# Kernel optimization log

Measured on AMD Instinct MI355X. Metric: run time of the kernel, lower is better.

## Reference

```python
import jax, jax.numpy as jnp
import numpy as np

N = 100000     # nodes
E = 1600000    # edges (avg degree 16)
CI = 3         # input features (x, z, t)
W = 128        # hidden width
CO = 1         # output features
L = 4          # processor layers


def setup_inputs() -> dict:
    key = jax.random.key(0)
    ks = jax.random.split(key, 10)
    s = 0.1
    x = jax.random.normal(ks[0], (N, CI), jnp.float32)
    # compute_mask is an external geometry-dependent, no-grad mask; emulate as 0/1 node mask
    mask = (jax.random.uniform(ks[1], (N, 1)) > 0.5).astype(jnp.float32)
    edge_index = jax.random.randint(ks[2], (2, E), 0, N, dtype=jnp.int32)
    W_enc = jax.random.normal(ks[3], (CI, W), jnp.float32) * s
    b_enc = jnp.zeros((W,), jnp.float32)
    W_p = jax.random.normal(ks[4], (L, W, W), jnp.float32) * s
    b_p = jnp.zeros((L, W), jnp.float32)
    W_dec = jax.random.normal(ks[5], (W, CO), jnp.float32) * s
    b_dec = jnp.zeros((CO,), jnp.float32)
    return {"x": x, "mask": mask, "edge_index": edge_index,
            "W_enc": W_enc, "b_enc": b_enc, "W_p": W_p, "b_p": b_p,
            "W_dec": W_dec, "b_dec": b_dec}


def reference(x, mask, edge_index, W_enc, b_enc, W_p, b_p, W_dec, b_dec):
    src, dst = edge_index[0], edge_index[1]
    n = x.shape[0]
    # GCN symmetric normalization with self-loops: deg = 1 + in-degree
    deg = 1.0 + jax.ops.segment_sum(jnp.ones((src.shape[0],), x.dtype), dst, num_segments=n)
    dis = jax.lax.rsqrt(deg)                      # deg^{-1/2}, [N]
    norm = dis[src] * dis[dst]                    # [E]

    def gcn(h, Wt, b):
        h = h @ Wt                                # [N, out]
        agg = jax.ops.segment_sum(h[src] * norm[:, None], dst, num_segments=n)
        # self-loop contribution: norm_ii = dis_i^2
        return agg + h * (dis * dis)[:, None] + b

    h = jax.nn.relu(gcn(x, W_enc, b_enc))
    for l in range(L):
        h = jax.nn.relu(gcn(h, W_p[l], b_p[l]))
    out = gcn(h, W_dec, b_dec)
    return out * mask
```

## Files before the change

kernel.cpp:

```cpp
#include <hip/hip_runtime.h>
#include <hip/hip_fp16.h>


#define HW 128
#define NBMAX 1024
#define CAP 4096
#define PBLK 256

typedef _Float16 f16x8 __attribute__((ext_vector_type(8)));
typedef float f32x4 __attribute__((ext_vector_type(4)));

__global__ void k_zero_i32(int* __restrict__ a, int n) {
    int i = blockIdx.x * 256 + threadIdx.x;
    if (i < n) a[i] = 0;
}

__global__ __launch_bounds__(256) void k_histb(const int* __restrict__ dstA,
                                               int* __restrict__ bcnt,
                                               int* __restrict__ pcnt,
                                               int nb, int e, int nblk) {
    __shared__ int lh[NBMAX];
    for (int b = threadIdx.x; b < nb; b += 256) lh[b] = 0;
    __syncthreads();
    int blk = blockIdx.x;
    int c0 = (int)(((long long)e * blk) / nblk);
    int c1 = (int)(((long long)e * (blk + 1)) / nblk);
    for (int i = c0 + threadIdx.x; i < c1; i += 256) atomicAdd(&lh[dstA[i] >> 7], 1);
    __syncthreads();
    for (int b = threadIdx.x; b < nb; b += 256) {
        int v = lh[b];
        pcnt[(size_t)blk * nb + b] = v;
        if (v) atomicAdd(&bcnt[b], v);
    }
}

__global__ void k_bscan(const int* __restrict__ bcnt, int* __restrict__ bstart,
                        int nb, int etot) {
    __shared__ int s[1024];
    int t = threadIdx.x;
    int d0 = (t < nb) ? bcnt[t] : 0;
    s[t] = d0;
    __syncthreads();
    for (int off = 1; off < 1024; off <<= 1) {
        int v = (t >= off) ? s[t - off] : 0;
        __syncthreads();
        s[t] += v;
        __syncthreads();
    }
    if (t < nb) bstart[t] = s[t] - d0;
    if (t == 0) bstart[nb] = etot;
}

__global__ __launch_bounds__(PBLK) void k_soff2(const int* __restrict__ pcnt,
                                                const int* __restrict__ bstart,
                                                int* __restrict__ soff, int nb) {
    __shared__ int s[PBLK];
    int b = blockIdx.x, t = threadIdx.x;
    int v = pcnt[(size_t)t * nb + b];
    s[t] = v;
    __syncthreads();
    for (int off = 1; off < PBLK; off <<= 1) {
        int u = (t >= off) ? s[t - off] : 0;
        __syncthreads();
        s[t] += u;
        __syncthreads();
    }
    soff[(size_t)t * nb + b] = bstart[b] + s[t] - v;
}

__global__ __launch_bounds__(256) void k_part(const int* __restrict__ srcA,
                                              const int* __restrict__ dstA,
                                              const int* __restrict__ soff,
                                              unsigned* __restrict__ stage,
                                              int nb, int e, int nblk) {
    __shared__ int loff[NBMAX];
    __shared__ int lh[NBMAX];
    int blk = blockIdx.x;
    for (int b = threadIdx.x; b < nb; b += 256) {
        loff[b] = soff[(size_t)blk * nb + b];
        lh[b] = 0;
    }
    __syncthreads();
    int c0 = (int)(((long long)e * blk) / nblk);
    int c1 = (int)(((long long)e * (blk + 1)) / nblk);
    for (int i = c0 + threadIdx.x; i < c1; i += 256) {
        int d = dstA[i];
        int bk = d >> 7;
        int p = loff[bk] + atomicAdd(&lh[bk], 1);
        stage[p] = ((unsigned)srcA[i] << 7) | (unsigned)(d & 127);
    }
}

__global__ __launch_bounds__(256) void k_build(const unsigned* __restrict__ stage,
                                               const int* __restrict__ bstart,
                                               const float* __restrict__ x,
                                               int* __restrict__ row_start,
                                               float* __restrict__ dis,
                                               float4* __restrict__ x4,
                                               int* __restrict__ csr, int n, int nb) {
    __shared__ int lcnt[128];
    __shared__ int sc[128];
    __shared__ int lcsr[CAP];
    int b = blockIdx.x, tid = threadIdx.x;
    int base = bstart[b], end = bstart[b + 1], cnt = end - base;
    int node0 = b << 7;

    if (tid < 128) lcnt[tid] = 0;
    __syncthreads();
    for (int j = tid; j < cnt; j += 256) atomicAdd(&lcnt[stage[base + j] & 127], 1);
    __syncthreads();
    if (tid < 128) sc[tid] = lcnt[tid];
    __syncthreads();
    for (int off = 1; off < 128; off <<= 1) {
        int v = (tid < 128 && tid >= off) ? sc[tid - off] : 0;
        __syncthreads();
        if (tid < 128) sc[tid] += v;
        __syncthreads();
    }
    int node = node0 + tid;
    if (tid < 128 && node < n) {
        int excl = sc[tid] - lcnt[tid];
        row_start[node] = base + excl;
        float dv = rsqrtf(1.f + (float)lcnt[tid]);
        dis[node] = dv;
        x4[node] = make_float4(x[node * 3] * dv, x[node * 3 + 1] * dv,
                               x[node * 3 + 2] * dv, 0.f);
    }
    if (tid == 0 && b == nb - 1) row_start[n] = end;
    __syncthreads();
    if (tid < 128) sc[tid] = sc[tid] - lcnt[tid];
    if (tid < 128) lcnt[tid] = 0;
    __syncthreads();
    if (cnt <= CAP) {
        for (int j = tid; j < cnt; j += 256) {
            unsigned v = stage[base + j];
            int dl = v & 127;
            int p = atomicAdd(&lcnt[dl], 1);
            lcsr[sc[dl] + p] = (int)(v >> 7);
        }
        __syncthreads();
        for (int j = tid; j < cnt; j += 256) csr[base + j] = lcsr[j];
    } else {
        for (int j = tid; j < cnt; j += 256) {
            unsigned v = stage[base + j];
            int dl = v & 127;
            int p = atomicAdd(&lcnt[dl], 1);
            csr[base + sc[dl] + p] = (int)(v >> 7);
        }
    }
}

__global__ void k_prep_wt(const float* __restrict__ Wp, __half* __restrict__ WTh,
                          __half* __restrict__ WTl, int total) {
    int t = blockIdx.x * 256 + threadIdx.x;
    if (t >= total) return;
    int l = t >> 14;
    int kc = t & 16383;
    int k = kc >> 7, c = kc & 127;
    float w = Wp[t];
    __half hi = __float2half_rn(w);
    __half lo = __float2half_rn(w - __half2float(hi));
    size_t o = ((size_t)l << 14) + (size_t)c * HW + k;
    WTh[o] = hi;
    WTl[o] = lo;
}

__global__ void k_enc_agg(const float4* __restrict__ x4, const int* __restrict__ rs,
                          const int* __restrict__ csr, const float* __restrict__ dis,
                          float4* __restrict__ zx, int n) {
    int i = blockIdx.x * 256 + threadIdx.x;
    if (i >= n) return;
    float4 a = x4[i];
    int e1 = rs[i + 1];
    for (int j = rs[i]; j < e1; ++j) {
        float4 v = x4[csr[j]];
        a.x += v.x; a.y += v.y; a.z += v.z;
    }
    float d = dis[i];
    zx[i] = make_float4(a.x * d, a.y * d, a.z * d, 0.f);
}

__global__ void k_enc_gemm(const float4* __restrict__ zx, const float* __restrict__ We,
                           const float* __restrict__ be, const float* __restrict__ dis,
                           __half* __restrict__ H, int n) {
    int t = blockIdx.x * 256 + threadIdx.x;
    int i = t >> 7;
    int c = t & 127;
    if (i >= n) return;
    float4 z = zx[i];
    float v = z.x * We[c] + z.y * We[HW + c] + z.z * We[2 * HW + c] + be[c];
    H[(size_t)i * HW + c] = __float2half_rn(fmaxf(v, 0.f) * dis[i]);
}

__global__ __launch_bounds__(256) void k_layer(const __half* __restrict__ Hin,
                                               const int* __restrict__ rs,
                                               const int* __restrict__ csr,
                                               const float* __restrict__ dis,
                                               const __half* __restrict__ WTh,
                                               const __half* __restrict__ WTl,
                                               const float* __restrict__ b,
                                               __half* __restrict__ Hout,
                                               const float* __restrict__ Wd,
                                               float* __restrict__ tout,
                                               int mode, int n) {
    __shared__ __half zs[16][136];
    __shared__ float psum[4][16];
    int wave = threadIdx.x >> 6, lane = threadIdx.x & 63;
    int lg = lane & 15;
    int ln = wave * 4 + (lane >> 4);
    int node = blockIdx.x * 16 + ln;
    bool active = node < n;

    float a0[8], a1[8], a2[8], a3[8];
#pragma unroll
    for (int j = 0; j < 8; ++j) { a0[j] = 0.f; a1[j] = 0.f; a2[j] = 0.f; a3[j] = 0.f; }

    int e0 = 0, e1 = 0;
    if (active) {
        e0 = rs[node];
        e1 = rs[node + 1];
        f16x8 hv = *(const f16x8*)(Hin + (size_t)node * HW + lg * 8);
#pragma unroll
        for (int j = 0; j < 8; ++j) a0[j] = (float)hv[j];
    }

    for (int base = e0; base < e1; base += 16) {
        int cnt = e1 - base;
        if (cnt > 16) cnt = 16;
        int sl = (base + lg < e1) ? csr[base + lg] : 0;
        int k = 0;
        for (; k + 4 <= cnt; k += 4) {
            int s0 = __shfl(sl, k + 0, 16);
            int s1 = __shfl(sl, k + 1, 16);
            int s2 = __shfl(sl, k + 2, 16);
            int s3 = __shfl(sl, k + 3, 16);
            f16x8 v0 = *(const f16x8*)(Hin + (size_t)s0 * HW + lg * 8);
            f16x8 v1 = *(const f16x8*)(Hin + (size_t)s1 * HW + lg * 8);
            f16x8 v2 = *(const f16x8*)(Hin + (size_t)s2 * HW + lg * 8);
            f16x8 v3 = *(const f16x8*)(Hin + (size_t)s3 * HW + lg * 8);
#pragma unroll
            for (int j = 0; j < 8; ++j) {
                a0[j] += (float)v0[j];
                a1[j] += (float)v1[j];
                a2[j] += (float)v2[j];
                a3[j] += (float)v3[j];
            }
        }
        for (; k < cnt; ++k) {
            int s = __shfl(sl, k, 16);
            f16x8 v = *(const f16x8*)(Hin + (size_t)s * HW + lg * 8);
#pragma unroll
            for (int j = 0; j < 8; ++j) a0[j] += (float)v[j];
        }
    }

    {
        float d = active ? dis[node] : 0.f;
        union { uint4 u; __half2 h[4]; } pk;
#pragma unroll
        for (int j = 0; j < 4; ++j) {
            float lo = d * ((a0[2 * j] + a1[2 * j]) + (a2[2 * j] + a3[2 * j]));
            float hi = d * ((a0[2 * j + 1] + a1[2 * j + 1]) + (a2[2 * j + 1] + a3[2 * j + 1]));
            pk.h[j] = __floats2half2_rn(lo, hi);
        }
        *(uint4*)&zs[ln][lg * 8] = pk.u;
    }
    __syncthreads();

    int q = lane >> 4, r16 = lane & 15;
    f32x4 acc[2];
    acc[0] = (f32x4)0.f;
    acc[1] = (f32x4)0.f;
#pragma unroll
    for (int ks = 0; ks < 4; ++ks) {
        f16x8 afr = *(const f16x8*)&zs[r16][ks * 32 + q * 8];
#pragma unroll
        for (int ntl = 0; ntl < 2; ++ntl) {
            int col = wave * 32 + ntl * 16 + r16;
            f16x8 bh = *(const f16x8*)(WTh + (size_t)col * HW + ks * 32 + q * 8);
            f16x8 bl = *(const f16x8*)(WTl + (size_t)col * HW + ks * 32 + q * 8);
            acc[ntl] = __builtin_amdgcn_mfma_f32_16x16x32_f16(afr, bh, acc[ntl], 0, 0, 0);
            acc[ntl] = __builtin_amdgcn_mfma_f32_16x16x32_f16(afr, bl, acc[ntl], 0, 0, 0);
        }
    }

    int row0 = blockIdx.x * 16;
    if (mode == 0) {
#pragma unroll
        for (int ntl = 0; ntl < 2; ++ntl) {
            int col = wave * 32 + ntl * 16 + r16;
            float bias = b[col];
#pragma unroll
            for (int r = 0; r < 4; ++r) {
                int row = row0 + q * 4 + r;
                if (row < n) {
                    float v = fmaxf(acc[ntl][r] + bias, 0.f) * dis[row];
                    Hout[(size_t)row * HW + col] = __float2half_rn(v);
                }
            }
        }
    } else {
        float pr[4];
#pragma unroll
        for (int r = 0; r < 4; ++r) pr[r] = 0.f;
#pragma unroll
        for (int ntl = 0; ntl < 2; ++ntl) {
            int col = wave * 32 + ntl * 16 + r16;
            float bias = b[col];
            float wd = Wd[col];
#pragma unroll
            for (int r = 0; r < 4; ++r)
                pr[r] += fmaxf(acc[ntl][r] + bias, 0.f) * wd;
        }
#pragma unroll
        for (int r = 0; r < 4; ++r) {
#pragma unroll
            for (int off = 1; off < 16; off <<= 1) pr[r] += __shfl_xor(pr[r], off, 16);
            if (r16 == 0) psum[wave][q * 4 + r] = pr[r];
        }
        __syncthreads();
        if (threadIdx.x < 16) {
            int row = row0 + threadIdx.x;
            if (row < n) {
                float t = (psum[0][threadIdx.x] + psum[1][threadIdx.x]) +
                          (psum[2][threadIdx.x] + psum[3][threadIdx.x]);
                tout[row] = t * dis[row];
            }
        }
    }
}

__global__ void k_dec_out(const float* __restrict__ t, const int* __restrict__ rs,
                          const int* __restrict__ csr, const float* __restrict__ dis,
                          const float* __restrict__ bdec, const float* __restrict__ mask,
                          float* __restrict__ out, int n) {
    int i = blockIdx.x * 256 + threadIdx.x;
    if (i >= n) return;
    float acc = t[i];
    int e1 = rs[i + 1];
    for (int j = rs[i]; j < e1; ++j) acc += t[csr[j]];
    out[i] = (dis[i] * acc + bdec[0]) * mask[i];
}

static inline size_t align256(size_t x) { return (x + 255) & ~(size_t)255; }

extern "C" void kernel_launch(void* const* d_in, const int* in_sizes, int n_in,
                              void* d_out, int out_size, void* d_ws, size_t ws_size,
                              hipStream_t stream) {
    const float* x     = (const float*)d_in[0];
    const float* mask  = (const float*)d_in[1];
    const int*   ei    = (const int*)d_in[2];
    const float* W_enc = (const float*)d_in[3];
    const float* b_enc = (const float*)d_in[4];
    const float* W_p   = (const float*)d_in[5];
    const float* b_p   = (const float*)d_in[6];
    const float* W_dec = (const float*)d_in[7];
    const float* b_dec = (const float*)d_in[8];

    const int N = in_sizes[1];
    const int E = in_sizes[2] / 2;
    const int* srcA = ei;
    const int* dstA = ei + E;
    const int NB = (N + 127) >> 7;

    char* p = (char*)d_ws;
    size_t off = 0;
    auto carve = [&](size_t bytes) {
        void* r = p + off;
        off += align256(bytes);
        return r;
    };
    int*      bcnt      = (int*)carve((size_t)NB * 4);
    int*      bstart    = (int*)carve((size_t)(NB + 1) * 4);
    int*      pcnt      = (int*)carve((size_t)PBLK * NB * 4);
    int*      soff      = (int*)carve((size_t)PBLK * NB * 4);
    int*      row_start = (int*)carve((size_t)(N + 1) * 4);
    unsigned* stage     = (unsigned*)carve((size_t)E * 4);
    int*      csr       = (int*)carve((size_t)E * 4);
    float*    dis       = (float*)carve((size_t)N * 4);
    float4*   x4        = (float4*)carve((size_t)N * 16);
    float4*   zx        = (float4*)carve((size_t)N * 16);
    float*    tdec      = (float*)carve((size_t)N * 4);
    __half*   WTh       = (__half*)carve((size_t)4 * HW * HW * 2);
    __half*   WTl       = (__half*)carve((size_t)4 * HW * HW * 2);
    __half*   HA        = (__half*)carve((size_t)N * HW * 2);
    __half*   HB        = (__half*)carve((size_t)N * HW * 2);

    const int gN   = (N + 255) / 256;
    const int gL   = (N + 15) / 16;
    const int WPT  = 4 * HW * HW;

    k_zero_i32<<<(NB + 255) / 256, 256, 0, stream>>>(bcnt, NB);
    k_histb<<<PBLK, 256, 0, stream>>>(dstA, bcnt, pcnt, NB, E, PBLK);
    k_bscan<<<1, 1024, 0, stream>>>(bcnt, bstart, NB, E);
    k_soff2<<<NB, PBLK, 0, stream>>>(pcnt, bstart, soff, NB);
    k_part<<<PBLK, 256, 0, stream>>>(srcA, dstA, soff, stage, NB, E, PBLK);
    k_build<<<NB, 256, 0, stream>>>(stage, bstart, x, row_start, dis, x4, csr, N, NB);
    k_prep_wt<<<(WPT + 255) / 256, 256, 0, stream>>>(W_p, WTh, WTl, WPT);

    k_enc_agg<<<gN, 256, 0, stream>>>(x4, row_start, csr, dis, zx, N);
    k_enc_gemm<<<(N * HW + 255) / 256, 256, 0, stream>>>(zx, W_enc, b_enc, dis, HA, N);

    __half* Hin = HA;
    __half* Hout = HB;
    for (int l = 0; l < 4; ++l) {
        int mode = (l == 3) ? 1 : 0;
        k_layer<<<gL, 256, 0, stream>>>(Hin, row_start, csr, dis,
                                        WTh + (size_t)l * HW * HW,
                                        WTl + (size_t)l * HW * HW,
                                        b_p + (size_t)l * HW, Hout,
                                        W_dec, tdec, mode, N);
        __half* t = Hin; Hin = Hout; Hout = t;
    }

    k_dec_out<<<gN, 256, 0, stream>>>(tdec, row_start, csr, dis, b_dec, mask,
                                      (float*)d_out, N);
}
```

Baseline: 506.8 us.

## Give each wave its own 16-node tile and full-width MFMA, drop block syncs

Each block now covers 64 nodes instead of 16. Each wave gathers 16 nodes in four sequential passes, writes them to a private LDS tile, and computes all 128 output columns with MFMA. Each wave therefore runs independently, and the __syncthreads plus the cross-wave psum reduction in the decoder path are removed. In exchange, each wave loads the full weight matrix (8 column tiles) rather than a quarter of it. The node gathers within a wave are serialized over four iterations, which reduces memory-level parallelism per wave, and register pressure rises from the 8 accumulators.

```diff
diff --git a/kernel.cpp b/kernel.cpp
--- a/kernel.cpp
+++ b/kernel.cpp
@@ -203,58 +203,55 @@
                                                const float* __restrict__ Wd,
                                                float* __restrict__ tout,
                                                int mode, int n) {
-    __shared__ __half zs[16][136];
-    __shared__ float psum[4][16];
+    __shared__ __half zs[4][16][136];
     int wave = threadIdx.x >> 6, lane = threadIdx.x & 63;
     int lg = lane & 15;
-    int ln = wave * 4 + (lane >> 4);
-    int node = blockIdx.x * 16 + ln;
-    bool active = node < n;
-
-    float a0[8], a1[8], a2[8], a3[8];
-#pragma unroll
-    for (int j = 0; j < 8; ++j) { a0[j] = 0.f; a1[j] = 0.f; a2[j] = 0.f; a3[j] = 0.f; }
-
-    int e0 = 0, e1 = 0;
-    if (active) {
-        e0 = rs[node];
-        e1 = rs[node + 1];
-        f16x8 hv = *(const f16x8*)(Hin + (size_t)node * HW + lg * 8);
-#pragma unroll
-        for (int j = 0; j < 8; ++j) a0[j] = (float)hv[j];
-    }
-
-    for (int base = e0; base < e1; base += 16) {
-        int cnt = e1 - base;
-        if (cnt > 16) cnt = 16;
-        int sl = (base + lg < e1) ? csr[base + lg] : 0;
-        int k = 0;
-        for (; k + 4 <= cnt; k += 4) {
-            int s0 = __shfl(sl, k + 0, 16);
-            int s1 = __shfl(sl, k + 1, 16);
-            int s2 = __shfl(sl, k + 2, 16);
-            int s3 = __shfl(sl, k + 3, 16);
-            f16x8 v0 = *(const f16x8*)(Hin + (size_t)s0 * HW + lg * 8);
-            f16x8 v1 = *(const f16x8*)(Hin + (size_t)s1 * HW + lg * 8);
-            f16x8 v2 = *(const f16x8*)(Hin + (size_t)s2 * HW + lg * 8);
-            f16x8 v3 = *(const f16x8*)(Hin + (size_t)s3 * HW + lg * 8);
-#pragma unroll
-            for (int j = 0; j < 8; ++j) {
-                a0[j] += (float)v0[j];
-                a1[j] += (float)v1[j];
-                a2[j] += (float)v2[j];
-                a3[j] += (float)v3[j];
+    int grp = lane >> 4;
+    int nodebase = blockIdx.x * 64 + wave * 16;
+
+    for (int t = 0; t < 4; ++t) {
+        int node = nodebase + t * 4 + grp;
+        bool active = node < n;
+        float a0[8], a1[8], a2[8], a3[8];
+#pragma unroll
+        for (int j = 0; j < 8; ++j) { a0[j] = 0.f; a1[j] = 0.f; a2[j] = 0.f; a3[j] = 0.f; }
+        int e0 = 0, e1 = 0;
+        if (active) {
+            e0 = rs[node];
+            e1 = rs[node + 1];
+            f16x8 hv = *(const f16x8*)(Hin + (size_t)node * HW + lg * 8);
+#pragma unroll
+            for (int j = 0; j < 8; ++j) a0[j] = (float)hv[j];
+        }
+        for (int base = e0; base < e1; base += 16) {
+            int cnt = e1 - base;
+            if (cnt > 16) cnt = 16;
+            int sl = (base + lg < e1) ? csr[base + lg] : 0;
+            int k = 0;
+            for (; k + 4 <= cnt; k += 4) {
+                int s0 = __shfl(sl, k + 0, 16);
+                int s1 = __shfl(sl, k + 1, 16);
+                int s2 = __shfl(sl, k + 2, 16);
+                int s3 = __shfl(sl, k + 3, 16);
+                f16x8 v0 = *(const f16x8*)(Hin + (size_t)s0 * HW + lg * 8);
+                f16x8 v1 = *(const f16x8*)(Hin + (size_t)s1 * HW + lg * 8);
+                f16x8 v2 = *(const f16x8*)(Hin + (size_t)s2 * HW + lg * 8);
+                f16x8 v3 = *(const f16x8*)(Hin + (size_t)s3 * HW + lg * 8);
+#pragma unroll
+                for (int j = 0; j < 8; ++j) {
+                    a0[j] += (float)v0[j];
+                    a1[j] += (float)v1[j];
+                    a2[j] += (float)v2[j];
+                    a3[j] += (float)v3[j];
+                }
             }
-        }
-        for (; k < cnt; ++k) {
-            int s = __shfl(sl, k, 16);
-            f16x8 v = *(const f16x8*)(Hin + (size_t)s * HW + lg * 8);
-#pragma unroll
-            for (int j = 0; j < 8; ++j) a0[j] += (float)v[j];
-        }
-    }
-
-    {
+            for (; k < cnt; ++k) {
+                int s = __shfl(sl, k, 16);
+                f16x8 v = *(const f16x8*)(Hin + (size_t)s * HW + lg * 8);
+#pragma unroll
+                for (int j = 0; j < 8; ++j) a0[j] += (float)v[j];
+            }
+        }
         float d = active ? dis[node] : 0.f;
         union { uint4 u; __half2 h[4]; } pk;
 #pragma unroll
@@ -263,68 +260,57 @@
             float hi = d * ((a0[2 * j + 1] + a1[2 * j + 1]) + (a2[2 * j + 1] + a3[2 * j + 1]));
             pk.h[j] = __floats2half2_rn(lo, hi);
         }
-        *(uint4*)&zs[ln][lg * 8] = pk.u;
-    }
-    __syncthreads();
+        *(uint4*)&zs[wave][t * 4 + grp][lg * 8] = pk.u;
+    }
 
     int q = lane >> 4, r16 = lane & 15;
-    f32x4 acc[2];
-    acc[0] = (f32x4)0.f;
-    acc[1] = (f32x4)0.f;
+    f32x4 acc[8];
+#pragma unroll
+    for (int nt = 0; nt < 8; ++nt) acc[nt] = (f32x4)0.f;
 #pragma unroll
     for (int ks = 0; ks < 4; ++ks) {
-        f16x8 afr = *(const f16x8*)&zs[r16][ks * 32 + q * 8];
-#pragma unroll
-        for (int ntl = 0; ntl < 2; ++ntl) {
-            int col = wave * 32 + ntl * 16 + r16;
-            f16x8 bh = *(const f16x8*)(WTh + (size_t)col * HW + ks * 32 + q * 8);
-            f16x8 bl = *(const f16x8*)(WTl + (size_t)col * HW + ks * 32 + q * 8);
-            acc[ntl] = __builtin_amdgcn_mfma_f32_16x16x32_f16(afr, bh, acc[ntl], 0, 0, 0);
-            acc[ntl] = __builtin_amdgcn_mfma_f32_16x16x32_f16(afr, bl, acc[ntl], 0, 0, 0);
-        }
-    }
-
-    int row0 = blockIdx.x * 16;
+        f16x8 afr = *(const f16x8*)&zs[wave][r16][ks * 32 + q * 8];
+#pragma unroll
+        for (int nt = 0; nt < 8; ++nt) {
+            f16x8 bh = *(const f16x8*)(WTh + (size_t)(nt * 16 + r16) * HW + ks * 32 + q * 8);
+            f16x8 bl = *(const f16x8*)(WTl + (size_t)(nt * 16 + r16) * HW + ks * 32 + q * 8);
+            acc[nt] = __builtin_amdgcn_mfma_f32_16x16x32_f16(afr, bh, acc[nt], 0, 0, 0);
+            acc[nt] = __builtin_amdgcn_mfma_f32_16x16x32_f16(afr, bl, acc[nt], 0, 0, 0);
+        }
+    }
+
     if (mode == 0) {
 #pragma unroll
-        for (int ntl = 0; ntl < 2; ++ntl) {
-            int col = wave * 32 + ntl * 16 + r16;
+        for (int nt = 0; nt < 8; ++nt) {
+            int col = nt * 16 + r16;
             float bias = b[col];
 #pragma unroll
             for (int r = 0; r < 4; ++r) {
-                int row = row0 + q * 4 + r;
+                int row = nodebase + q * 4 + r;
                 if (row < n) {
-                    float v = fmaxf(acc[ntl][r] + bias, 0.f) * dis[row];
+                    float v = fmaxf(acc[nt][r] + bias, 0.f) * dis[row];
                     Hout[(size_t)row * HW + col] = __float2half_rn(v);
                 }
             }
         }
     } else {
-        float pr[4];
-#pragma unroll
-        for (int r = 0; r < 4; ++r) pr[r] = 0.f;
-#pragma unroll
-        for (int ntl = 0; ntl < 2; ++ntl) {
-            int col = wave * 32 + ntl * 16 + r16;
+        float pr[4] = {0.f, 0.f, 0.f, 0.f};
+#pragma unroll
+        for (int nt = 0; nt < 8; ++nt) {
+            int col = nt * 16 + r16;
             float bias = b[col];
             float wd = Wd[col];
 #pragma unroll
             for (int r = 0; r < 4; ++r)
-                pr[r] += fmaxf(acc[ntl][r] + bias, 0.f) * wd;
+                pr[r] += fmaxf(acc[nt][r] + bias, 0.f) * wd;
         }
 #pragma unroll
         for (int r = 0; r < 4; ++r) {
 #pragma unroll
             for (int off = 1; off < 16; off <<= 1) pr[r] += __shfl_xor(pr[r], off, 16);
-            if (r16 == 0) psum[wave][q * 4 + r] = pr[r];
-        }
-        __syncthreads();
-        if (threadIdx.x < 16) {
-            int row = row0 + threadIdx.x;
-            if (row < n) {
-                float t = (psum[0][threadIdx.x] + psum[1][threadIdx.x]) +
-                          (psum[2][threadIdx.x] + psum[3][threadIdx.x]);
-                tout[row] = t * dis[row];
+            if (r16 == 0) {
+                int row = nodebase + q * 4 + r;
+                if (row < n) tout[row] = pr[r] * dis[row];
             }
         }
     }
@@ -387,7 +373,7 @@
     __half*   HB        = (__half*)carve((size_t)N * HW * 2);
 
     const int gN   = (N + 255) / 256;
-    const int gL   = (N + 15) / 16;
+    const int gL   = (N + 63) / 64;
     const int WPT  = 4 * HW * HW;
 
     k_zero_i32<<<(NB + 255) / 256, 256, 0, stream>>>(bcnt, NB);
```

Result: slower. 604.9 us (+19.4%).
